# Performance work log

Measured on AMD Instinct MI355X. Metric: run time of the kernel, lower is better.

The kernel has to match this reference:

```python
import jax, jax.numpy as jnp
import numpy as np

PRESERVE_RATIO = 0.8
TEMPERATURE = 1.5


def setup_inputs() -> dict:
    key = jax.random.key(0)
    ks = jax.random.split(key, 8)
    B, C, H, W = 2, 64, 96, 96
    inter = C // 2
    bott = C // 4
    s = 0.02
    return {
        "x": jax.random.normal(ks[0], (B, C, H, W), dtype=jnp.float32),
        "g_w": jax.random.normal(ks[1], (inter, C), dtype=jnp.float32) * s,
        "theta_w": jax.random.normal(ks[2], (inter, C), dtype=jnp.float32) * s,
        "phi_w": jax.random.normal(ks[3], (inter, C), dtype=jnp.float32) * s,
        "W_w": jax.random.normal(ks[4], (C, inter), dtype=jnp.float32) * s,
        "cg1_w": jax.random.normal(ks[5], (bott, C), dtype=jnp.float32) * s,
        "cg1_b": jnp.zeros((bott,), dtype=jnp.float32),
        "cg2_w": jax.random.normal(ks[6], (C, bott), dtype=jnp.float32) * s,
        "cg2_b": jnp.zeros((C,), dtype=jnp.float32),
    }


def reference(x, g_w, theta_w, phi_w, W_w, cg1_w, cg1_b, cg2_w, cg2_b):
    B, C, H, W = x.shape
    N = H * W
    # color gate: global avg pool -> 1x1 conv -> relu -> 1x1 conv -> sigmoid
    pooled = jnp.mean(x, axis=(2, 3))                       # [B, C]
    h = jax.nn.relu(pooled @ cg1_w.T + cg1_b)               # [B, C//4]
    gate = jax.nn.sigmoid(h @ cg2_w.T + cg2_b)              # [B, C]

    xf = x.reshape(B, C, N)                                 # [B, C, N]
    g_x = jnp.einsum('ic,bcn->bni', g_w, xf)                # [B, N, I]
    theta = jnp.einsum('ic,bcn->bni', theta_w, xf)          # [B, N, I]
    phi = jnp.einsum('ic,bcn->bin', phi_w, xf)              # [B, I, N]

    affinity = jnp.einsum('bni,bim->bnm', theta, phi) / TEMPERATURE  # [B, N, N]
    affinity = jax.nn.softmax(affinity, axis=-1)
    y = jnp.einsum('bnm,bmi->bni', affinity, g_x)           # [B, N, I]
    y = jnp.einsum('ci,bni->bcn', W_w, y).reshape(B, C, H, W)
    y = y * gate[:, :, None, None] * PRESERVE_RATIO
    return x + y
```

## Files before the change

### kernel.cpp

```cpp
#include <hip/hip_runtime.h>

#define N_TOK 9216
#define C_DIM 64
#define I_DIM 32
#define BOT 16
#define B_SZ 2
#define N_TILES 144

typedef short bf16x8 __attribute__((ext_vector_type(8)));
typedef float f32x4 __attribute__((ext_vector_type(4)));
typedef float f32x16 __attribute__((ext_vector_type(16)));

__device__ __forceinline__ unsigned packbf(float a, float b) {
  return __builtin_amdgcn_perm(__float_as_uint(b), __float_as_uint(a), 0x07060302u);
}
__device__ __forceinline__ unsigned short bftrunc(float f) {
  return (unsigned short)(__float_as_uint(f) >> 16);
}

__global__ __launch_bounds__(256) void proj_pool_kernel(
    const float* __restrict__ x, const float* __restrict__ g_w,
    const float* __restrict__ theta_w, const float* __restrict__ phi_w,
    unsigned short* __restrict__ Q, unsigned short* __restrict__ K,
    unsigned short* __restrict__ VT, float* __restrict__ pooled) {
  if (blockIdx.x >= 864) {
    int bc = blockIdx.x - 864;
    const float* p = x + (size_t)bc * N_TOK;
    float s = 0.f;
    for (int t = threadIdx.x; t < N_TOK; t += 256) s += p[t];
#pragma unroll
    for (int off = 32; off >= 1; off >>= 1) s += __shfl_down(s, off, 64);
    __shared__ float red[4];
    int wid = threadIdx.x >> 6, lane = threadIdx.x & 63;
    if (lane == 0) red[wid] = s;
    __syncthreads();
    if (threadIdx.x == 0)
      pooled[bc] = (red[0] + red[1] + red[2] + red[3]) * (1.0f / N_TOK);
    return;
  }
  const int lane = threadIdx.x & 63;
  const int m = lane & 15, quad = lane >> 4;
  int task = blockIdx.x * 4 + (threadIdx.x >> 6);
  int mat = task / 1152;
  int r0 = task % 1152;
  int b = r0 / 576;
  int n0 = (r0 % 576) * 16;
  const float* wsrc = (mat == 0) ? theta_w : ((mat == 1) ? phi_w : g_w);
  const float scale = (mat == 0) ? 0.96179669439f : 1.0f;

  bf16x8 afr[2][2];
#pragma unroll
  for (int it = 0; it < 2; ++it)
#pragma unroll
    for (int cs = 0; cs < 2; ++cs) {
      const float* wp = wsrc + (it * 16 + m) * C_DIM + cs * 32 + quad * 8;
      union { unsigned u[4]; bf16x8 v; } t;
#pragma unroll
      for (int j = 0; j < 4; ++j)
        t.u[j] = packbf(wp[2 * j] * scale, wp[2 * j + 1] * scale);
      afr[it][cs] = t.v;
    }

  const float* xb = x + (size_t)b * C_DIM * N_TOK + n0 + m;
  bf16x8 bfr[2];
#pragma unroll
  for (int cs = 0; cs < 2; ++cs) {
    union { unsigned u[4]; bf16x8 v; } t;
#pragma unroll
    for (int j = 0; j < 4; ++j) {
      float v0 = xb[(size_t)(cs * 32 + quad * 8 + 2 * j) * N_TOK];
      float v1 = xb[(size_t)(cs * 32 + quad * 8 + 2 * j + 1) * N_TOK];
      t.u[j] = packbf(v0, v1);
    }
    bfr[cs] = t.v;
  }

  f32x4 acc[2] = {{0.f, 0.f, 0.f, 0.f}, {0.f, 0.f, 0.f, 0.f}};
#pragma unroll
  for (int cs = 0; cs < 2; ++cs)
#pragma unroll
    for (int it = 0; it < 2; ++it)
      acc[it] = __builtin_amdgcn_mfma_f32_16x16x32_bf16(afr[it][cs], bfr[cs],
                                                        acc[it], 0, 0, 0);
  if (mat < 2) {
    unsigned short* dst =
        ((mat == 0) ? Q : K) + ((size_t)b * N_TOK + n0 + m) * I_DIM;
#pragma unroll
    for (int it = 0; it < 2; ++it) {
      unsigned u0 = packbf(acc[it][0], acc[it][1]);
      unsigned u1 = packbf(acc[it][2], acc[it][3]);
      *(uint2*)(dst + it * 16 + quad * 4) = make_uint2(u0, u1);
    }
  } else {
#pragma unroll
    for (int it = 0; it < 2; ++it)
#pragma unroll
      for (int r = 0; r < 4; ++r)
        VT[((size_t)b * I_DIM + it * 16 + quad * 4 + r) * N_TOK + n0 + m] =
            bftrunc(acc[it][r]);
  }
}

__device__ __forceinline__ void tilework(const f32x16 s, const bf16x8 bvA,
                                         const bf16x8 bvB, f32x16& accy,
                                         float& lsum) {
  float e[16];
#pragma unroll
  for (int r = 0; r < 16; ++r) e[r] = __builtin_amdgcn_exp2f(s[r]);
  float l0 = 0.f, l1 = 0.f, l2 = 0.f, l3 = 0.f;
#pragma unroll
  for (int r = 0; r < 4; ++r) {
    l0 += e[r]; l1 += e[4 + r]; l2 += e[8 + r]; l3 += e[12 + r];
  }
  lsum += (l0 + l1) + (l2 + l3);
  unsigned pk[8];
#pragma unroll
  for (int i = 0; i < 8; ++i) pk[i] = packbf(e[2 * i], e[2 * i + 1]);
  asm("v_permlane32_swap_b32 %0, %1" : "+v"(pk[0]), "+v"(pk[2]));
  asm("v_permlane32_swap_b32 %0, %1" : "+v"(pk[1]), "+v"(pk[3]));
  asm("v_permlane32_swap_b32 %0, %1" : "+v"(pk[4]), "+v"(pk[6]));
  asm("v_permlane32_swap_b32 %0, %1" : "+v"(pk[5]), "+v"(pk[7]));
  union { unsigned u[4]; bf16x8 v; } A0, A1;
  A0.u[0] = pk[0]; A0.u[1] = pk[1]; A0.u[2] = pk[2]; A0.u[3] = pk[3];
  A1.u[0] = pk[4]; A1.u[1] = pk[5]; A1.u[2] = pk[6]; A1.u[3] = pk[7];
  accy = __builtin_amdgcn_mfma_f32_32x32x16_bf16(A0.v, bvA, accy, 0, 0, 0);
  accy = __builtin_amdgcn_mfma_f32_32x32x16_bf16(A1.v, bvB, accy, 0, 0, 0);
}

__device__ __forceinline__ void attn_step(const bf16x8 bq0, const bf16x8 bq1,
                                          bf16x8 cak[4], bf16x8 cbv[4],
                                          bf16x8 nak[4], bf16x8 nbv[4],
                                          const unsigned short*& kp,
                                          const unsigned short*& vp,
                                          f32x16& accy, float& lsum) {
  const f32x16 zz = {};
  kp += 64 * I_DIM;
  vp += 64;
  nak[0] = *(const bf16x8*)(kp);
  nak[1] = *(const bf16x8*)(kp + 16);
  nak[2] = *(const bf16x8*)(kp + 32 * I_DIM);
  nak[3] = *(const bf16x8*)(kp + 32 * I_DIM + 16);
  nbv[0] = *(const bf16x8*)(vp);
  nbv[1] = *(const bf16x8*)(vp + 16);
  nbv[2] = *(const bf16x8*)(vp + 32);
  nbv[3] = *(const bf16x8*)(vp + 48);

  f32x16 s0 = __builtin_amdgcn_mfma_f32_32x32x16_bf16(cak[0], bq0, zz, 0, 0, 0);
  s0 = __builtin_amdgcn_mfma_f32_32x32x16_bf16(cak[1], bq1, s0, 0, 0, 0);
  f32x16 s1 = __builtin_amdgcn_mfma_f32_32x32x16_bf16(cak[2], bq0, zz, 0, 0, 0);
  s1 = __builtin_amdgcn_mfma_f32_32x32x16_bf16(cak[3], bq1, s1, 0, 0, 0);

  tilework(s0, cbv[0], cbv[1], accy, lsum);
  tilework(s1, cbv[2], cbv[3], accy, lsum);
}

__global__ __launch_bounds__(256, 4) void attn_kernel(
    const unsigned short* __restrict__ Q, const unsigned short* __restrict__ Kg,
    const unsigned short* __restrict__ VT, float* __restrict__ Ypart,
    float* __restrict__ Lpart, int tps) {
  const int lane = threadIdx.x & 63;
  const int l32 = lane & 31, h = lane >> 5;
  const int qw = blockIdx.x * 4 + (threadIdx.x >> 6);
  const int ks = blockIdx.y, b = blockIdx.z;
  const int q0 = qw * 32;
  const unsigned short* Qb = Q + (size_t)b * N_TOK * I_DIM;
  const unsigned short* Kb = Kg + (size_t)b * N_TOK * I_DIM;
  const unsigned short* Vb = VT + (size_t)b * I_DIM * N_TOK;

  bf16x8 bq0 = *(const bf16x8*)(Qb + (size_t)(q0 + l32) * I_DIM + h * 8);
  bf16x8 bq1 = *(const bf16x8*)(Qb + (size_t)(q0 + l32) * I_DIM + 16 + h * 8);

  f32x16 accy = {};
  float lsum = 0.f;

  const int kt0 = ks * tps;
  const unsigned short* kp = Kb + ((size_t)kt0 * 64 + l32) * I_DIM + h * 8;
  const unsigned short* vp = Vb + (size_t)l32 * N_TOK + kt0 * 64 + h * 8;

  bf16x8 ak[4], bv[4], nak[4], nbv[4];
  ak[0] = *(const bf16x8*)(kp);
  ak[1] = *(const bf16x8*)(kp + 16);
  ak[2] = *(const bf16x8*)(kp + 32 * I_DIM);
  ak[3] = *(const bf16x8*)(kp + 32 * I_DIM + 16);
  bv[0] = *(const bf16x8*)(vp);
  bv[1] = *(const bf16x8*)(vp + 16);
  bv[2] = *(const bf16x8*)(vp + 32);
  bv[3] = *(const bf16x8*)(vp + 48);

  const int half = tps >> 1;
  for (int it = 0; it < half; ++it) {
    attn_step(bq0, bq1, ak, bv, nak, nbv, kp, vp, accy, lsum);
    attn_step(bq0, bq1, nak, nbv, ak, bv, kp, vp, accy, lsum);
  }

  lsum += __shfl_xor(lsum, 32, 64);

  const size_t base = (size_t)(ks * B_SZ + b) * N_TOK + q0;
#pragma unroll
  for (int R = 0; R < 4; ++R)
#pragma unroll
    for (int r = 0; r < 4; ++r)
      Ypart[(base + r + 8 * R + 4 * h) * I_DIM + l32] = accy[4 * R + r];
  if (h == 0) Lpart[base + l32] = lsum;
}

__global__ __launch_bounds__(256) void epilogue_kernel(
    const float* __restrict__ x, const float* __restrict__ W_w,
    const float* __restrict__ pooled, const float* __restrict__ cg1_w,
    const float* __restrict__ cg1_b, const float* __restrict__ cg2_w,
    const float* __restrict__ cg2_b, const float* __restrict__ Ypart,
    const float* __restrict__ Lpart, float* __restrict__ out, int KS) {
  __shared__ float Ysh[64][33];
  __shared__ float lsh[64];
  __shared__ float gsh[64];
  __shared__ float hl[BOT];
  const int t = threadIdx.x;
  const int b = blockIdx.y;
  const int n0 = blockIdx.x * 64;

  if (t < BOT) {
    float a = cg1_b[t];
#pragma unroll
    for (int c = 0; c < C_DIM; ++c)
      a += cg1_w[t * C_DIM + c] * pooled[b * C_DIM + c];
    hl[t] = a > 0.f ? a : 0.f;
  }

  {
    int nl = t >> 2, i0 = (t & 3) * 8;
    float4 s0 = make_float4(0.f, 0.f, 0.f, 0.f), s1 = s0;
    for (int ks = 0; ks < KS; ++ks) {
      const float* yp =
          Ypart + ((size_t)(ks * B_SZ + b) * N_TOK + n0 + nl) * I_DIM + i0;
      float4 v0 = *(const float4*)(yp);
      float4 v1 = *(const float4*)(yp + 4);
      s0.x += v0.x; s0.y += v0.y; s0.z += v0.z; s0.w += v0.w;
      s1.x += v1.x; s1.y += v1.y; s1.z += v1.z; s1.w += v1.w;
    }
    Ysh[nl][i0 + 0] = s0.x; Ysh[nl][i0 + 1] = s0.y;
    Ysh[nl][i0 + 2] = s0.z; Ysh[nl][i0 + 3] = s0.w;
    Ysh[nl][i0 + 4] = s1.x; Ysh[nl][i0 + 5] = s1.y;
    Ysh[nl][i0 + 6] = s1.z; Ysh[nl][i0 + 7] = s1.w;
    if (t < 64) {
      float ls = 0.f;
      for (int ks = 0; ks < KS; ++ks)
        ls += Lpart[(size_t)(ks * B_SZ + b) * N_TOK + n0 + t];
      lsh[t] = ls;
    }
  }
  __syncthreads();

  if (t < C_DIM) {
    float z = cg2_b[t];
#pragma unroll
    for (int j = 0; j < BOT; ++j) z += cg2_w[t * BOT + j] * hl[j];
    gsh[t] = 0.8f / (1.f + __expf(-z));
  }
  __syncthreads();

  const int n = t & 63, cg = t >> 6;
  float y[I_DIM];
#pragma unroll
  for (int i = 0; i < I_DIM; ++i) y[i] = Ysh[n][i];
  const float inv = 1.0f / lsh[n];
  const float* xb = x + ((size_t)b * C_DIM + cg * 16) * N_TOK + n0 + n;
  float* ob = out + ((size_t)b * C_DIM + cg * 16) * N_TOK + n0 + n;
#pragma unroll
  for (int c16 = 0; c16 < 16; ++c16) {
    const int c = cg * 16 + c16;
    float sacc = 0.f;
#pragma unroll
    for (int i = 0; i < I_DIM; ++i) sacc += W_w[c * I_DIM + i] * y[i];
    ob[(size_t)c16 * N_TOK] = xb[(size_t)c16 * N_TOK] + gsh[c] * inv * sacc;
  }
}

extern "C" void kernel_launch(void* const* d_in, const int* in_sizes, int n_in,
                              void* d_out, int out_size, void* d_ws, size_t ws_size,
                              hipStream_t stream) {
  const float* x = (const float*)d_in[0];
  const float* g_w = (const float*)d_in[1];
  const float* theta_w = (const float*)d_in[2];
  const float* phi_w = (const float*)d_in[3];
  const float* W_w = (const float*)d_in[4];
  const float* cg1_w = (const float*)d_in[5];
  const float* cg1_b = (const float*)d_in[6];
  const float* cg2_w = (const float*)d_in[7];
  const float* cg2_b = (const float*)d_in[8];
  float* out = (float*)d_out;

  char* w = (char*)d_ws;
  const size_t bfsz = (size_t)B_SZ * N_TOK * I_DIM * sizeof(unsigned short);
  unsigned short* Qb = (unsigned short*)(w);
  unsigned short* Kb = (unsigned short*)(w + bfsz);
  unsigned short* VT = (unsigned short*)(w + 2 * bfsz);
  float* pooled = (float*)(w + 3 * bfsz);
  char* w2 = w + 3 * bfsz + 4096;

  int KS = 8;
  {
    const size_t per = (size_t)B_SZ * N_TOK * sizeof(float) * (I_DIM + 1);
    while (KS > 1 && (3 * bfsz + 4096 + (size_t)KS * per) > ws_size) KS >>= 1;
  }
  float* Lpart = (float*)w2;
  float* Ypart = (float*)(w2 + (size_t)KS * B_SZ * N_TOK * sizeof(float));
  int tps = N_TILES / KS;

  proj_pool_kernel<<<dim3(992), 256, 0, stream>>>(x, g_w, theta_w, phi_w, Qb,
                                                  Kb, VT, pooled);
  attn_kernel<<<dim3(72, KS, B_SZ), 256, 0, stream>>>(Qb, Kb, VT, Ypart, Lpart, tps);
  epilogue_kernel<<<dim3(N_TOK / 64, B_SZ), 256, 0, stream>>>(
      x, W_w, pooled, cg1_w, cg1_b, cg2_w, cg2_b, Ypart, Lpart, out, KS);
}
```

Before: 176.3 us.

## Store attention partials as bf16 and double key-split count

Attention partial outputs are written as truncated bf16 instead of fp32, halving partial-buffer traffic into the epilogue, which now unpacks bf16 pairs. The key-split factor rises from 8 to 16, doubling the attention grid for more parallelism at the cost of more partials to reduce. The ping-pong double-buffered step is replaced by a simple loop that prefetches only K, with V loaded inside each iteration. Truncating partials adds rounding error to the accumulated output.

```diff
diff --git a/kernel.cpp b/kernel.cpp
--- a/kernel.cpp
+++ b/kernel.cpp
@@ -16,6 +16,12 @@
 }
 __device__ __forceinline__ unsigned short bftrunc(float f) {
   return (unsigned short)(__float_as_uint(f) >> 16);
+}
+__device__ __forceinline__ float bflo(unsigned u) {
+  return __uint_as_float(u << 16);
+}
+__device__ __forceinline__ float bfhi(unsigned u) {
+  return __uint_as_float(u & 0xffff0000u);
 }
 
 __global__ __launch_bounds__(256) void proj_pool_kernel(
@@ -127,36 +133,16 @@
   accy = __builtin_amdgcn_mfma_f32_32x32x16_bf16(A1.v, bvB, accy, 0, 0, 0);
 }
 
-__device__ __forceinline__ void attn_step(const bf16x8 bq0, const bf16x8 bq1,
-                                          bf16x8 cak[4], bf16x8 cbv[4],
-                                          bf16x8 nak[4], bf16x8 nbv[4],
-                                          const unsigned short*& kp,
-                                          const unsigned short*& vp,
-                                          f32x16& accy, float& lsum) {
-  const f32x16 zz = {};
-  kp += 64 * I_DIM;
-  vp += 64;
-  nak[0] = *(const bf16x8*)(kp);
-  nak[1] = *(const bf16x8*)(kp + 16);
-  nak[2] = *(const bf16x8*)(kp + 32 * I_DIM);
-  nak[3] = *(const bf16x8*)(kp + 32 * I_DIM + 16);
-  nbv[0] = *(const bf16x8*)(vp);
-  nbv[1] = *(const bf16x8*)(vp + 16);
-  nbv[2] = *(const bf16x8*)(vp + 32);
-  nbv[3] = *(const bf16x8*)(vp + 48);
-
-  f32x16 s0 = __builtin_amdgcn_mfma_f32_32x32x16_bf16(cak[0], bq0, zz, 0, 0, 0);
-  s0 = __builtin_amdgcn_mfma_f32_32x32x16_bf16(cak[1], bq1, s0, 0, 0, 0);
-  f32x16 s1 = __builtin_amdgcn_mfma_f32_32x32x16_bf16(cak[2], bq0, zz, 0, 0, 0);
-  s1 = __builtin_amdgcn_mfma_f32_32x32x16_bf16(cak[3], bq1, s1, 0, 0, 0);
-
-  tilework(s0, cbv[0], cbv[1], accy, lsum);
-  tilework(s1, cbv[2], cbv[3], accy, lsum);
+__device__ __forceinline__ void loadK(bf16x8 a[4], const unsigned short* kp) {
+  a[0] = *(const bf16x8*)(kp);
+  a[1] = *(const bf16x8*)(kp + 16);
+  a[2] = *(const bf16x8*)(kp + 32 * I_DIM);
+  a[3] = *(const bf16x8*)(kp + 32 * I_DIM + 16);
 }
 
 __global__ __launch_bounds__(256, 4) void attn_kernel(
     const unsigned short* __restrict__ Q, const unsigned short* __restrict__ Kg,
-    const unsigned short* __restrict__ VT, float* __restrict__ Ypart,
+    const unsigned short* __restrict__ VT, unsigned short* __restrict__ Ypart,
     float* __restrict__ Lpart, int tps) {
   const int lane = threadIdx.x & 63;
   const int l32 = lane & 31, h = lane >> 5;
@@ -175,22 +161,30 @@
 
   const int kt0 = ks * tps;
   const unsigned short* kp = Kb + ((size_t)kt0 * 64 + l32) * I_DIM + h * 8;
-  const unsigned short* vp = Vb + (size_t)l32 * N_TOK + kt0 * 64 + h * 8;
-
-  bf16x8 ak[4], bv[4], nak[4], nbv[4];
-  ak[0] = *(const bf16x8*)(kp);
-  ak[1] = *(const bf16x8*)(kp + 16);
-  ak[2] = *(const bf16x8*)(kp + 32 * I_DIM);
-  ak[3] = *(const bf16x8*)(kp + 32 * I_DIM + 16);
-  bv[0] = *(const bf16x8*)(vp);
-  bv[1] = *(const bf16x8*)(vp + 16);
-  bv[2] = *(const bf16x8*)(vp + 32);
-  bv[3] = *(const bf16x8*)(vp + 48);
-
-  const int half = tps >> 1;
-  for (int it = 0; it < half; ++it) {
-    attn_step(bq0, bq1, ak, bv, nak, nbv, kp, vp, accy, lsum);
-    attn_step(bq0, bq1, nak, nbv, ak, bv, kp, vp, accy, lsum);
+  const unsigned short* vp0 = Vb + (size_t)l32 * N_TOK + kt0 * 64 + h * 8;
+
+  const f32x16 zz = {};
+  bf16x8 ak[4];
+  loadK(ak, kp);
+  for (int kt = 0; kt < tps; ++kt) {
+    kp += 64 * I_DIM;
+    bf16x8 nak[4];
+    loadK(nak, kp);
+    const unsigned short* vp = vp0 + kt * 64;
+    bf16x8 bv0 = *(const bf16x8*)(vp);
+    bf16x8 bv1 = *(const bf16x8*)(vp + 16);
+    bf16x8 bv2 = *(const bf16x8*)(vp + 32);
+    bf16x8 bv3 = *(const bf16x8*)(vp + 48);
+
+    f32x16 s0 = __builtin_amdgcn_mfma_f32_32x32x16_bf16(ak[0], bq0, zz, 0, 0, 0);
+    s0 = __builtin_amdgcn_mfma_f32_32x32x16_bf16(ak[1], bq1, s0, 0, 0, 0);
+    f32x16 s1 = __builtin_amdgcn_mfma_f32_32x32x16_bf16(ak[2], bq0, zz, 0, 0, 0);
+    s1 = __builtin_amdgcn_mfma_f32_32x32x16_bf16(ak[3], bq1, s1, 0, 0, 0);
+
+    tilework(s0, bv0, bv1, accy, lsum);
+    tilework(s1, bv2, bv3, accy, lsum);
+
+    ak[0] = nak[0]; ak[1] = nak[1]; ak[2] = nak[2]; ak[3] = nak[3];
   }
 
   lsum += __shfl_xor(lsum, 32, 64);
@@ -200,7 +194,7 @@
   for (int R = 0; R < 4; ++R)
 #pragma unroll
     for (int r = 0; r < 4; ++r)
-      Ypart[(base + r + 8 * R + 4 * h) * I_DIM + l32] = accy[4 * R + r];
+      Ypart[(base + r + 8 * R + 4 * h) * I_DIM + l32] = bftrunc(accy[4 * R + r]);
   if (h == 0) Lpart[base + l32] = lsum;
 }
 
@@ -208,7 +202,7 @@
     const float* __restrict__ x, const float* __restrict__ W_w,
     const float* __restrict__ pooled, const float* __restrict__ cg1_w,
     const float* __restrict__ cg1_b, const float* __restrict__ cg2_w,
-    const float* __restrict__ cg2_b, const float* __restrict__ Ypart,
+    const float* __restrict__ cg2_b, const unsigned short* __restrict__ Ypart,
     const float* __restrict__ Lpart, float* __restrict__ out, int KS) {
   __shared__ float Ysh[64][33];
   __shared__ float lsh[64];
@@ -228,19 +222,20 @@
 
   {
     int nl = t >> 2, i0 = (t & 3) * 8;
-    float4 s0 = make_float4(0.f, 0.f, 0.f, 0.f), s1 = s0;
+    float s[8];
+#pragma unroll
+    for (int k = 0; k < 8; ++k) s[k] = 0.f;
     for (int ks = 0; ks < KS; ++ks) {
-      const float* yp =
+      const unsigned short* yp =
           Ypart + ((size_t)(ks * B_SZ + b) * N_TOK + n0 + nl) * I_DIM + i0;
-      float4 v0 = *(const float4*)(yp);
-      float4 v1 = *(const float4*)(yp + 4);
-      s0.x += v0.x; s0.y += v0.y; s0.z += v0.z; s0.w += v0.w;
-      s1.x += v1.x; s1.y += v1.y; s1.z += v1.z; s1.w += v1.w;
-    }
-    Ysh[nl][i0 + 0] = s0.x; Ysh[nl][i0 + 1] = s0.y;
-    Ysh[nl][i0 + 2] = s0.z; Ysh[nl][i0 + 3] = s0.w;
-    Ysh[nl][i0 + 4] = s1.x; Ysh[nl][i0 + 5] = s1.y;
-    Ysh[nl][i0 + 6] = s1.z; Ysh[nl][i0 + 7] = s1.w;
+      uint4 v = *(const uint4*)yp;
+      s[0] += bflo(v.x); s[1] += bfhi(v.x);
+      s[2] += bflo(v.y); s[3] += bfhi(v.y);
+      s[4] += bflo(v.z); s[5] += bfhi(v.z);
+      s[6] += bflo(v.w); s[7] += bfhi(v.w);
+    }
+#pragma unroll
+    for (int k = 0; k < 8; ++k) Ysh[nl][i0 + k] = s[k];
     if (t < 64) {
       float ls = 0.f;
       for (int ks = 0; ks < KS; ++ks)
@@ -295,15 +290,16 @@
   unsigned short* Kb = (unsigned short*)(w + bfsz);
   unsigned short* VT = (unsigned short*)(w + 2 * bfsz);
   float* pooled = (float*)(w + 3 * bfsz);
-  char* w2 = w + 3 * bfsz + 4096;
-
-  int KS = 8;
+  char* w2 = w + 3 * bfsz + 8192;
+
+  int KS = 16;
   {
-    const size_t per = (size_t)B_SZ * N_TOK * sizeof(float) * (I_DIM + 1);
-    while (KS > 1 && (3 * bfsz + 4096 + (size_t)KS * per) > ws_size) KS >>= 1;
+    const size_t per = (size_t)B_SZ * N_TOK * (I_DIM * 2 + 4);
+    while (KS > 1 && (3 * bfsz + 8192 + (size_t)KS * per) > ws_size) KS >>= 1;
   }
   float* Lpart = (float*)w2;
-  float* Ypart = (float*)(w2 + (size_t)KS * B_SZ * N_TOK * sizeof(float));
+  unsigned short* Ypart =
+      (unsigned short*)(w2 + (size_t)KS * B_SZ * N_TOK * sizeof(float));
   int tps = N_TILES / KS;
 
   proj_pool_kernel<<<dim3(992), 256, 0, stream>>>(x, g_w, theta_w, phi_w, Qb,
```

Result: no change. 175.4 us (-0.5%).
